# Performance work log

Hardware: AMD Instinct MI355X
Metric: run time of the kernel (lower is better)

The kernel has to match this reference:

```python
import jax, jax.numpy as jnp
import numpy as np


def _nearest(x, cb):
    # x: [N, D], cb: [K, D]. Squared euclidean distances (same argmin as cdist).
    d2 = (jnp.sum(x * x, axis=-1, keepdims=True)
          - 2.0 * (x @ cb.T)
          + jnp.sum(cb * cb, axis=-1))
    idx = jnp.argmin(d2, axis=-1)
    return cb[idx]


def pq_quantize(w, codebook, row_scale, D):
    # w: [O, I], codebook: [K, D], row_scale: [O, 1]
    O, I = w.shape
    w_scaled = w / row_scale
    groups = w_scaled.reshape(-1, D)            # [O*I/D, D]
    q = _nearest(groups, codebook)              # [O*I/D, D]
    return q.reshape(O, I) * row_scale


def setup_inputs() -> dict:
    key = jax.random.key(0)
    kU, kB, kcU, kcB = jax.random.split(key, 4)
    K, r, d, D, K_cb = 32768, 256, 1024, 8, 256
    U = jax.random.normal(kU, (K, r), dtype=jnp.float32)
    B = jax.random.normal(kB, (r, d), dtype=jnp.float32)
    rs_U = jnp.clip(jnp.max(jnp.abs(U), axis=1, keepdims=True), 1e-6)
    rs_B = jnp.clip(jnp.max(jnp.abs(B), axis=1, keepdims=True), 1e-6)
    cb_U = jax.random.normal(kcU, (K_cb, D), dtype=jnp.float32)
    cb_B = jax.random.normal(kcB, (K_cb, D), dtype=jnp.float32)
    return {"U": U, "B": B, "rs_U": rs_U, "rs_B": rs_B,
            "cb_U": cb_U, "cb_B": cb_B, "D": D}


def reference(U, B, rs_U, rs_B, cb_U, cb_B, D):
    Uq = pq_quantize(U, cb_U, rs_U, D)   # [K, r]
    Bq = pq_quantize(B, cb_B, rs_B, D)   # [r, d]
    return Uq @ Bq                       # all_rows(): [K, d]
```

## Files before the change

### kernel.cpp

```cpp
#include <hip/hip_runtime.h>
#include <math.h>

#define CB_K 256
#define PQ_D 8

typedef __attribute__((ext_vector_type(2))) float f32x2;
typedef __attribute__((ext_vector_type(4))) float f32x4;
typedef __attribute__((ext_vector_type(8))) short bf16x8;

__device__ __forceinline__ ushort f2bf(float f) {
    unsigned u = __float_as_uint(f);
    unsigned r = (u + 0x7FFFu + ((u >> 16) & 1u)) >> 16;
    return (ushort)r;
}
__device__ __forceinline__ float bf2f(ushort h) {
    return __uint_as_float(((unsigned)h) << 16);
}

template <int LOG2_GPR>
__global__ __launch_bounds__(256)
void pq_quant_split(const float* __restrict__ w, const float* __restrict__ cb,
                    const float* __restrict__ rs,
                    ushort* __restrict__ oh, ushort* __restrict__ ol)
{
    __shared__ float s_cb[CB_K * PQ_D];
    __shared__ float s_cb2[CB_K];
    const int t = threadIdx.x;
    for (int i = t; i < CB_K * PQ_D; i += 256) s_cb[i] = cb[i];
    __syncthreads();
    {
        float s = 0.f;
#pragma unroll
        for (int j = 0; j < PQ_D; j++) { float c = s_cb[t * PQ_D + j]; s += c * c; }
        s_cb2[t] = s;
    }
    __syncthreads();

    const int gbase = blockIdx.x * 1024;
    f32x2 xm2[4][4];
    float sc[4], best[4];
    int   bi[4];
#pragma unroll
    for (int j = 0; j < 4; j++) {
        const int g = gbase + j * 256 + t;
        sc[j] = rs[g >> LOG2_GPR];
        const float4* wp = (const float4*)(w + (size_t)g * PQ_D);
        float4 a = wp[0], b = wp[1];
        xm2[j][0] = f32x2{-2.f * a.x, -2.f * a.y};
        xm2[j][1] = f32x2{-2.f * a.z, -2.f * a.w};
        xm2[j][2] = f32x2{-2.f * b.x, -2.f * b.y};
        xm2[j][3] = f32x2{-2.f * b.z, -2.f * b.w};
        best[j] = INFINITY; bi[j] = 0;
    }

    for (int k = 0; k < CB_K; k++) {
        const float4 c01 = *(const float4*)(s_cb + k * PQ_D);
        const float4 c23 = *(const float4*)(s_cb + k * PQ_D + 4);
        const float  cc  = s_cb2[k];
        const f32x2 c0{c01.x, c01.y}, c1{c01.z, c01.w}, c2{c23.x, c23.y}, c3{c23.z, c23.w};
#pragma unroll
        for (int j = 0; j < 4; j++) {
            f32x2 acc = xm2[j][0] * c0;
            acc += xm2[j][1] * c1;
            acc += xm2[j][2] * c2;
            acc += xm2[j][3] * c3;
            float val = fmaf(sc[j], cc, acc.x + acc.y);
            bool p = val < best[j];
            best[j] = p ? val : best[j];
            bi[j]   = p ? k : bi[j];
        }
    }

#pragma unroll
    for (int j = 0; j < 4; j++) {
        const int g = gbase + j * 256 + t;
        const float4* cp = (const float4*)(s_cb + bi[j] * PQ_D);
        float4 q0 = cp[0], q1 = cp[1];
        float v[8] = {q0.x, q0.y, q0.z, q0.w, q1.x, q1.y, q1.z, q1.w};
        bf16x8 vh, vl;
#pragma unroll
        for (int e = 0; e < 8; e++) {
            float f = v[e] * sc[j];
            ushort h = f2bf(f);
            vh[e] = (short)h;
            vl[e] = (short)f2bf(f - bf2f(h));
        }
        *(bf16x8*)(oh + (size_t)g * PQ_D) = vh;
        *(bf16x8*)(ol + (size_t)g * PQ_D) = vl;
    }
}

__global__ __launch_bounds__(256)
void pq_quant_split_T(const float* __restrict__ w, const float* __restrict__ cb,
                      const float* __restrict__ rs,
                      ushort* __restrict__ oh, ushort* __restrict__ ol,
                      int log2_gpr, int O)
{
    __shared__ float s_cb[CB_K * PQ_D];
    __shared__ float s_cb2[CB_K];
    const int t = threadIdx.x;
    for (int i = t; i < CB_K * PQ_D; i += 256) s_cb[i] = cb[i];
    __syncthreads();
    {
        float s = 0.f;
#pragma unroll
        for (int j = 0; j < PQ_D; j++) { float c = s_cb[t * PQ_D + j]; s += c * c; }
        s_cb2[t] = s;
    }
    __syncthreads();

    const int g = blockIdx.x * 256 + t;
    const int gpr_mask = (1 << log2_gpr) - 1;
    const int row  = g >> log2_gpr;
    const int col0 = (g & gpr_mask) * PQ_D;
    const float s = rs[row];

    const float4* wp = (const float4*)(w + (size_t)g * PQ_D);
    float4 a = wp[0], b = wp[1];
    f32x2 xm2[4] = {f32x2{-2.f * a.x, -2.f * a.y}, f32x2{-2.f * a.z, -2.f * a.w},
                    f32x2{-2.f * b.x, -2.f * b.y}, f32x2{-2.f * b.z, -2.f * b.w}};
    float best = INFINITY; int bi = 0;
    for (int k = 0; k < CB_K; k++) {
        const float4 c01 = *(const float4*)(s_cb + k * PQ_D);
        const float4 c23 = *(const float4*)(s_cb + k * PQ_D + 4);
        f32x2 acc = xm2[0] * f32x2{c01.x, c01.y};
        acc += xm2[1] * f32x2{c01.z, c01.w};
        acc += xm2[2] * f32x2{c23.x, c23.y};
        acc += xm2[3] * f32x2{c23.z, c23.w};
        float val = fmaf(s, s_cb2[k], acc.x + acc.y);
        bool p = val < best;
        best = p ? val : best;
        bi   = p ? k : bi;
    }

    const float4* cp = (const float4*)(s_cb + bi * PQ_D);
    float4 q0 = cp[0], q1 = cp[1];
    float v[8] = {q0.x, q0.y, q0.z, q0.w, q1.x, q1.y, q1.z, q1.w};
#pragma unroll
    for (int e = 0; e < 8; e++) {
        float f = v[e] * s;
        ushort h = f2bf(f);
        oh[(size_t)(col0 + e) * O + row] = h;
        ol[(size_t)(col0 + e) * O + row] = f2bf(f - bf2f(h));
    }
}

#define BM 128
#define BN 128
#define BK 64

__device__ __forceinline__ void gl_lds16(const void* g, void* l) {
    __builtin_amdgcn_global_load_lds((const __attribute__((address_space(1))) void*)g,
                                     (__attribute__((address_space(3))) void*)l, 16, 0, 0);
}

__global__ __launch_bounds__(256, 2)
void gemm3(const ushort* __restrict__ Ah, const ushort* __restrict__ Al,
           const ushort* __restrict__ Bh, const ushort* __restrict__ Bl,
           float* __restrict__ C, int M, int N, int K)
{
    __shared__ __align__(16) ushort sAh[BM * BK], sAl[BM * BK];
    __shared__ __align__(16) ushort sBh[BN * BK], sBl[BN * BK];

    const int t    = threadIdx.x;
    const int lane = t & 63;
    const int wv   = t >> 6;
    const int wr = wv >> 1, wc = wv & 1;
    const int l15 = lane & 15, kq = lane >> 4;
    const int bm = blockIdx.y * BM, bn = blockIdx.x * BN;

    int srow[4], sslot[4];
#pragma unroll
    for (int r = 0; r < 4; r++) {
        int n = r * 4096 + t * 16;
        int row = n >> 7;
        int slot = ((n >> 4) & 7) ^ (row & 7);
        srow[r] = row; sslot[r] = slot;
    }

    f32x4 acc[4][4];
#pragma unroll
    for (int i = 0; i < 4; i++)
#pragma unroll
        for (int j = 0; j < 4; j++) acc[i][j] = f32x4{0.f, 0.f, 0.f, 0.f};

    const char* pAh = (const char*)Ah;
    const char* pAl = (const char*)Al;
    const char* pBh = (const char*)Bh;
    const char* pBl = (const char*)Bl;

    for (int ks = 0; ks < K / BK; ks++) {
        const int k0 = ks * BK;
        if (ks) __syncthreads();
#pragma unroll
        for (int r = 0; r < 4; r++) {
            size_t offA = ((size_t)(bm + srow[r]) * K + k0 + sslot[r] * 8) * 2;
            size_t offB = ((size_t)(bn + srow[r]) * K + k0 + sslot[r] * 8) * 2;
            int ldso = r * 4096 + wv * 1024;
            gl_lds16(pAh + offA, (char*)sAh + ldso);
            gl_lds16(pAl + offA, (char*)sAl + ldso);
            gl_lds16(pBh + offB, (char*)sBh + ldso);
            gl_lds16(pBl + offB, (char*)sBl + ldso);
        }
        __syncthreads();

#pragma unroll
        for (int kk = 0; kk < 2; kk++) {
            bf16x8 ah[4], al[4], bh[4], bl[4];
#pragma unroll
            for (int f = 0; f < 4; f++) {
                int mr = wr * 64 + f * 16 + l15;
                int offa = mr * 128 + (((kk * 4 + kq) ^ (mr & 7)) * 16);
                ah[f] = *(const bf16x8*)((const char*)sAh + offa);
                al[f] = *(const bf16x8*)((const char*)sAl + offa);
                int nr = wc * 64 + f * 16 + l15;
                int offb = nr * 128 + (((kk * 4 + kq) ^ (nr & 7)) * 16);
                bh[f] = *(const bf16x8*)((const char*)sBh + offb);
                bl[f] = *(const bf16x8*)((const char*)sBl + offb);
            }
#pragma unroll
            for (int mf = 0; mf < 4; mf++)
#pragma unroll
                for (int nf = 0; nf < 4; nf++) {
                    acc[mf][nf] = __builtin_amdgcn_mfma_f32_16x16x32_bf16(ah[mf], bh[nf], acc[mf][nf], 0, 0, 0);
                    acc[mf][nf] = __builtin_amdgcn_mfma_f32_16x16x32_bf16(ah[mf], bl[nf], acc[mf][nf], 0, 0, 0);
                    acc[mf][nf] = __builtin_amdgcn_mfma_f32_16x16x32_bf16(al[mf], bh[nf], acc[mf][nf], 0, 0, 0);
                }
        }
    }

#pragma unroll
    for (int mf = 0; mf < 4; mf++) {
        const int r0 = bm + wr * 64 + mf * 16 + kq * 4;
#pragma unroll
        for (int nf = 0; nf < 4; nf++) {
            const int cc = bn + wc * 64 + nf * 16 + l15;
#pragma unroll
            for (int rr = 0; rr < 4; rr++)
                C[(size_t)(r0 + rr) * N + cc] = acc[mf][nf][rr];
        }
    }
}

extern "C" void kernel_launch(void* const* d_in, const int* in_sizes, int n_in,
                              void* d_out, int out_size, void* d_ws, size_t ws_size,
                              hipStream_t stream)
{
    const float* U    = (const float*)d_in[0];
    const float* B    = (const float*)d_in[1];
    const float* rs_U = (const float*)d_in[2];
    const float* rs_B = (const float*)d_in[3];
    const float* cb_U = (const float*)d_in[4];
    const float* cb_B = (const float*)d_in[5];
    float* out = (float*)d_out;

    const int M = 32768, K = 256, N = 1024;

    ushort* Ahi  = (ushort*)d_ws;
    ushort* Alo  = Ahi + (size_t)M * K;
    ushort* BThi = Alo + (size_t)M * K;
    ushort* BTlo = BThi + (size_t)N * K;

    pq_quant_split<5><<<1024, 256, 0, stream>>>(U, cb_U, rs_U, Ahi, Alo);
    pq_quant_split_T<<<128, 256, 0, stream>>>(B, cb_B, rs_B, BThi, BTlo, 7, K);

    dim3 grid(N / BN, M / BM);
    gemm3<<<grid, 256, 0, stream>>>(Ahi, Alo, BThi, BTlo, out, M, N, K);
}
```

Baseline: 299.8 us.

## Compute U codebook distances with bf16x3 MFMA and remap GEMM blocks per XCD

The U quantization kernel stops computing per-thread fp32 dot products over all 256 codewords. It builds an error-compensated bf16 (hi/mid/lo) split of the codebook, its squared norms and the scaled inputs, then computes the distance scores with 16x16x32 bf16 MFMAs, followed by a wave-level argmin via shuffles. The GEMM launch becomes a 1D grid whose block index is remapped so that consecutive M tiles land on the same XCD, aiming for better L2 reuse of the B operand. The triple-bf16 split targets near-fp32 distance accuracy, but rounding could still flip argmin ties relative to the reference. The remap also hardcodes grid shape assumptions (8 N tiles, 2048 blocks).

```diff
diff --git a/kernel.cpp b/kernel.cpp
--- a/kernel.cpp
+++ b/kernel.cpp
@@ -7,6 +7,7 @@
 typedef __attribute__((ext_vector_type(2))) float f32x2;
 typedef __attribute__((ext_vector_type(4))) float f32x4;
 typedef __attribute__((ext_vector_type(8))) short bf16x8;
+typedef __attribute__((ext_vector_type(4))) unsigned int u32x4;
 
 __device__ __forceinline__ ushort f2bf(float f) {
     unsigned u = __float_as_uint(f);
@@ -16,77 +17,122 @@
 __device__ __forceinline__ float bf2f(ushort h) {
     return __uint_as_float(((unsigned)h) << 16);
 }
-
-template <int LOG2_GPR>
+__device__ __forceinline__ unsigned pk2(ushort lo, ushort hi) {
+    return (unsigned)lo | ((unsigned)hi << 16);
+}
+
 __global__ __launch_bounds__(256)
-void pq_quant_split(const float* __restrict__ w, const float* __restrict__ cb,
-                    const float* __restrict__ rs,
-                    ushort* __restrict__ oh, ushort* __restrict__ ol)
+void pq_quant_mfma_u(const float* __restrict__ w, const float* __restrict__ cb,
+                     const float* __restrict__ rs,
+                     ushort* __restrict__ oh, ushort* __restrict__ ol)
 {
-    __shared__ float s_cb[CB_K * PQ_D];
-    __shared__ float s_cb2[CB_K];
+    __shared__ ushort A_lds[CB_K][40];
+
     const int t = threadIdx.x;
-    for (int i = t; i < CB_K * PQ_D; i += 256) s_cb[i] = cb[i];
+
+    {
+        const float* cp = cb + t * PQ_D;
+        float v[9]; float cc = 0.f;
+#pragma unroll
+        for (int j = 0; j < 8; j++) { float c = cp[j]; v[j] = c; cc += c * c; }
+        v[8] = cc;
+        ushort hh[9], mm[9], ll[9];
+#pragma unroll
+        for (int j = 0; j < 9; j++) {
+            float x = v[j];
+            ushort h = f2bf(x); float r  = x - bf2f(h);
+            ushort m = f2bf(r); float r2 = r - bf2f(m);
+            hh[j] = h; mm[j] = m; ll[j] = f2bf(r2);
+        }
+        *(u32x4*)&A_lds[t][0]  = u32x4{pk2(hh[0],hh[1]), pk2(hh[2],hh[3]), pk2(hh[4],hh[5]), pk2(hh[6],hh[7])};
+        *(u32x4*)&A_lds[t][8]  = u32x4{pk2(mm[0],mm[1]), pk2(mm[2],mm[3]), pk2(mm[4],mm[5]), pk2(mm[6],mm[7])};
+        *(u32x4*)&A_lds[t][16] = u32x4{pk2(ll[0],ll[1]), pk2(ll[2],ll[3]), pk2(ll[4],ll[5]), pk2(ll[6],ll[7])};
+        *(u32x4*)&A_lds[t][24] = u32x4{pk2(hh[8],mm[8]), pk2(ll[8],0), 0u, 0u};
+    }
     __syncthreads();
-    {
-        float s = 0.f;
-#pragma unroll
-        for (int j = 0; j < PQ_D; j++) { float c = s_cb[t * PQ_D + j]; s += c * c; }
-        s_cb2[t] = s;
-    }
-    __syncthreads();
-
-    const int gbase = blockIdx.x * 1024;
-    f32x2 xm2[4][4];
-    float sc[4], best[4];
-    int   bi[4];
-#pragma unroll
-    for (int j = 0; j < 4; j++) {
-        const int g = gbase + j * 256 + t;
-        sc[j] = rs[g >> LOG2_GPR];
+
+    const int lane = t & 63;
+    const int wv   = t >> 6;
+    const int l15  = lane & 15;
+    const int kq   = lane >> 4;
+    const int kq4  = kq * 4;
+    const int gw   = blockIdx.x * 4 + wv;
+
+    for (int it = 0; it < 16; it++) {
+        const int tile = gw * 16 + it;
+        const int g    = tile * 16 + l15;
+        const float s  = rs[g >> 5];
+
         const float4* wp = (const float4*)(w + (size_t)g * PQ_D);
-        float4 a = wp[0], b = wp[1];
-        xm2[j][0] = f32x2{-2.f * a.x, -2.f * a.y};
-        xm2[j][1] = f32x2{-2.f * a.z, -2.f * a.w};
-        xm2[j][2] = f32x2{-2.f * b.x, -2.f * b.y};
-        xm2[j][3] = f32x2{-2.f * b.z, -2.f * b.w};
-        best[j] = INFINITY; bi[j] = 0;
-    }
-
-    for (int k = 0; k < CB_K; k++) {
-        const float4 c01 = *(const float4*)(s_cb + k * PQ_D);
-        const float4 c23 = *(const float4*)(s_cb + k * PQ_D + 4);
-        const float  cc  = s_cb2[k];
-        const f32x2 c0{c01.x, c01.y}, c1{c01.z, c01.w}, c2{c23.x, c23.y}, c3{c23.z, c23.w};
-#pragma unroll
-        for (int j = 0; j < 4; j++) {
-            f32x2 acc = xm2[j][0] * c0;
-            acc += xm2[j][1] * c1;
-            acc += xm2[j][2] * c2;
-            acc += xm2[j][3] * c3;
-            float val = fmaf(sc[j], cc, acc.x + acc.y);
-            bool p = val < best[j];
-            best[j] = p ? val : best[j];
-            bi[j]   = p ? k : bi[j];
-        }
-    }
-
-#pragma unroll
-    for (int j = 0; j < 4; j++) {
-        const int g = gbase + j * 256 + t;
-        const float4* cp = (const float4*)(s_cb + bi[j] * PQ_D);
-        float4 q0 = cp[0], q1 = cp[1];
-        float v[8] = {q0.x, q0.y, q0.z, q0.w, q1.x, q1.y, q1.z, q1.w};
-        bf16x8 vh, vl;
-#pragma unroll
-        for (int e = 0; e < 8; e++) {
-            float f = v[e] * sc[j];
-            ushort h = f2bf(f);
-            vh[e] = (short)h;
-            vl[e] = (short)f2bf(f - bf2f(h));
-        }
-        *(bf16x8*)(oh + (size_t)g * PQ_D) = vh;
-        *(bf16x8*)(ol + (size_t)g * PQ_D) = vl;
+        float4 wa = wp[0], wb = wp[1];
+        float u[8] = {-2.f*wa.x, -2.f*wa.y, -2.f*wa.z, -2.f*wa.w,
+                      -2.f*wb.x, -2.f*wb.y, -2.f*wb.z, -2.f*wb.w};
+        ushort uh[8], um[8], ul[8];
+#pragma unroll
+        for (int j = 0; j < 8; j++) {
+            ushort h = f2bf(u[j]); float r  = u[j] - bf2f(h);
+            ushort m = f2bf(r);    float r2 = r - bf2f(m);
+            uh[j] = h; um[j] = m; ul[j] = f2bf(r2);
+        }
+        ushort sh = f2bf(s); float sr = s - bf2f(sh);
+        ushort sm = f2bf(sr); ushort sl = f2bf(sr - bf2f(sm));
+
+        u32x4 Ph{pk2(uh[0],uh[1]), pk2(uh[2],uh[3]), pk2(uh[4],uh[5]), pk2(uh[6],uh[7])};
+        u32x4 Pm{pk2(um[0],um[1]), pk2(um[2],um[3]), pk2(um[4],um[5]), pk2(um[6],um[7])};
+        u32x4 Pl{pk2(ul[0],ul[1]), pk2(ul[2],ul[3]), pk2(ul[4],ul[5]), pk2(ul[6],ul[7])};
+        u32x4 Z{0u,0u,0u,0u};
+        u32x4 S1{pk2(sh,sh), pk2(sh,0), 0u, 0u};
+        u32x4 S2{pk2(sm,sm), 0u, 0u, 0u};
+        u32x4 S3{pk2(sl,0), 0u, 0u, 0u};
+
+        u32x4 w1 = (kq == 3) ? S1 : Ph;
+        u32x4 w2 = (kq == 3) ? S2 : ((kq <= 1) ? Pm : Z);
+        u32x4 w3 = (kq == 3) ? S3 : ((kq == 0) ? Pl : Z);
+
+        bf16x8 b1 = __builtin_bit_cast(bf16x8, w1);
+        bf16x8 b2 = __builtin_bit_cast(bf16x8, w2);
+        bf16x8 b3 = __builtin_bit_cast(bf16x8, w3);
+
+        float best = INFINITY;
+        int   bidx = 0;
+#pragma unroll
+        for (int mt = 0; mt < 16; mt++) {
+            bf16x8 a = *(const bf16x8*)&A_lds[mt * 16 + l15][kq4 * 2];
+            f32x4 acc{0.f, 0.f, 0.f, 0.f};
+            acc = __builtin_amdgcn_mfma_f32_16x16x32_bf16(a, b1, acc, 0, 0, 0);
+            acc = __builtin_amdgcn_mfma_f32_16x16x32_bf16(a, b2, acc, 0, 0, 0);
+            acc = __builtin_amdgcn_mfma_f32_16x16x32_bf16(a, b3, acc, 0, 0, 0);
+#pragma unroll
+            for (int r = 0; r < 4; r++) {
+                int kk = mt * 16 + r + kq4;
+                bool p = acc[r] < best;
+                best = p ? acc[r] : best;
+                bidx = p ? kk : bidx;
+            }
+        }
+#pragma unroll
+        for (int msk = 16; msk <= 32; msk <<= 1) {
+            float ob = __shfl_xor(best, msk);
+            int   oi = __shfl_xor(bidx, msk);
+            bool p = (ob < best) || (ob == best && oi < bidx);
+            best = p ? ob : best;
+            bidx = p ? oi : bidx;
+        }
+        if (kq == 0) {
+            const float4* cp2 = (const float4*)(cb + bidx * PQ_D);
+            float4 c0 = cp2[0], c1 = cp2[1];
+            float y[8] = {c0.x*s, c0.y*s, c0.z*s, c0.w*s, c1.x*s, c1.y*s, c1.z*s, c1.w*s};
+            ushort yh[8], yl[8];
+#pragma unroll
+            for (int j = 0; j < 8; j++) {
+                ushort h = f2bf(y[j]);
+                yh[j] = h; yl[j] = f2bf(y[j] - bf2f(h));
+            }
+            *(u32x4*)(oh + (size_t)g * PQ_D) =
+                u32x4{pk2(yh[0],yh[1]), pk2(yh[2],yh[3]), pk2(yh[4],yh[5]), pk2(yh[6],yh[7])};
+            *(u32x4*)(ol + (size_t)g * PQ_D) =
+                u32x4{pk2(yl[0],yl[1]), pk2(yl[2],yl[3]), pk2(yl[4],yl[5]), pk2(yl[6],yl[7])};
+        }
     }
 }
 
@@ -167,7 +213,13 @@
     const int wv   = t >> 6;
     const int wr = wv >> 1, wc = wv & 1;
     const int l15 = lane & 15, kq = lane >> 4;
-    const int bm = blockIdx.y * BM, bn = blockIdx.x * BN;
+
+    const int h   = blockIdx.x;
+    const int xcd = h & 7;
+    const int tt  = h >> 3;
+    const int bn_i = tt & 7, bm8 = tt >> 3;
+    const int bm = (bm8 * 8 + xcd) * BM;
+    const int bn = bn_i * BN;
 
     int srow[4], sslot[4];
 #pragma unroll
@@ -261,9 +313,8 @@
     ushort* BThi = Alo + (size_t)M * K;
     ushort* BTlo = BThi + (size_t)N * K;
 
-    pq_quant_split<5><<<1024, 256, 0, stream>>>(U, cb_U, rs_U, Ahi, Alo);
+    pq_quant_mfma_u<<<1024, 256, 0, stream>>>(U, cb_U, rs_U, Ahi, Alo);
     pq_quant_split_T<<<128, 256, 0, stream>>>(B, cb_B, rs_B, BThi, BTlo, 7, K);
 
-    dim3 grid(N / BN, M / BM);
-    gemm3<<<grid, 256, 0, stream>>>(Ahi, Alo, BThi, BTlo, out, M, N, K);
-}
+    gemm3<<<2048, 256, 0, stream>>>(Ahi, Alo, BThi, BTlo, out, M, N, K);
+}
```

After: 293.3 us. 1.02x faster.
